# Performance work log

Hardware: AMD Instinct MI355X
Metric: run time of the kernel (lower is better)

## Reference

```python
import jax, jax.numpy as jnp
import numpy as np

B, S, D, H = 4, 2048, 1024, 16
HS = D // H          # head size 64
DF = 4 * D           # ffn hidden 4096
EPS = 1e-5


def _layer_norm(x, g, b):
    mu = jnp.mean(x, axis=-1, keepdims=True)
    var = jnp.var(x, axis=-1, keepdims=True)
    return (x - mu) * jax.lax.rsqrt(var + EPS) * g + b


def setup_inputs() -> dict:
    key = jax.random.key(0)
    ks = jax.random.split(key, 12)
    s_d = 1.0 / np.sqrt(D)
    s_f = 1.0 / np.sqrt(DF)
    return {
        "x": jax.random.normal(ks[0], (B, S, D), jnp.float32),
        # per-head q/k/v projections, batched over heads: [H, D, HS]
        "wq": jax.random.uniform(ks[1], (H, D, HS), jnp.float32, -s_d, s_d),
        "wk": jax.random.uniform(ks[2], (H, D, HS), jnp.float32, -s_d, s_d),
        "wv": jax.random.uniform(ks[3], (H, D, HS), jnp.float32, -s_d, s_d),
        "proj_w": jax.random.uniform(ks[4], (D, D), jnp.float32, -s_d, s_d),
        "proj_b": jax.random.uniform(ks[5], (D,), jnp.float32, -s_d, s_d),
        "ff1_w": jax.random.uniform(ks[6], (D, DF), jnp.float32, -s_d, s_d),
        "ff1_b": jax.random.uniform(ks[7], (DF,), jnp.float32, -s_d, s_d),
        "ff2_w": jax.random.uniform(ks[8], (DF, D), jnp.float32, -s_f, s_f),
        "ff2_b": jax.random.uniform(ks[9], (D,), jnp.float32, -s_f, s_f),
        "ln1_g": jnp.ones((D,), jnp.float32),
        "ln1_b": jnp.zeros((D,), jnp.float32),
        "ln2_g": jnp.ones((D,), jnp.float32),
        "ln2_b": jnp.zeros((D,), jnp.float32),
    }


def reference(x, wq, wk, wv, proj_w, proj_b, ff1_w, ff1_b, ff2_w, ff2_b,
              ln1_g, ln1_b, ln2_g, ln2_b):
    # --- multi-head causal self-attention on ln1(x), all heads batched ---
    h = _layer_norm(x, ln1_g, ln1_b)                      # [B,S,D]
    q = jnp.einsum("bsd,hde->bhse", h, wq)                # [B,H,S,HS]
    k = jnp.einsum("bsd,hde->bhse", h, wk)
    v = jnp.einsum("bsd,hde->bhse", h, wv)
    scale = HS ** -0.5
    scores = jnp.einsum("bhse,bhte->bhst", q, k) * scale  # [B,H,S,S]
    causal = jnp.tril(jnp.ones((S, S), bool))
    scores = jnp.where(causal, scores, jnp.finfo(scores.dtype).min)
    att = jax.nn.softmax(scores, axis=-1)
    o = jnp.einsum("bhst,bhte->bhse", att, v)             # [B,H,S,HS]
    o = o.transpose(0, 2, 1, 3).reshape(B, S, D)          # concat heads
    sa = o @ proj_w + proj_b
    x = x + sa
    # --- FFN on ln2(x) ---
    h2 = _layer_norm(x, ln2_g, ln2_b)
    ff = jax.nn.relu(h2 @ ff1_w + ff1_b) @ ff2_w + ff2_b
    return x + ff
```

## Files before the change

kernel.cpp:

```cpp
#include <hip/hip_runtime.h>
#include <hip/hip_bf16.h>

#define BB 4
#define SS 2048
#define DD 1024
#define HH 16
#define HSZ 64
#define DFF 4096

typedef short short8 __attribute__((ext_vector_type(8)));
typedef float f32x4 __attribute__((ext_vector_type(4)));
typedef unsigned short us4 __attribute__((ext_vector_type(4)));

#define AS1 __attribute__((address_space(1)))
#define AS3 __attribute__((address_space(3)))

__device__ __forceinline__ unsigned short f2bf(float f) {
    return __bfloat16_as_ushort(__float2bfloat16(f));
}

__global__ __launch_bounds__(256) void pack_qkv_kernel(
    const float* __restrict__ wq, const float* __restrict__ wk,
    const float* __restrict__ wv, __hip_bfloat16* __restrict__ out)
{
    int id = blockIdx.x * 256 + threadIdx.x;
    int n = id >> 10;
    int k = id & 1023;
    int sel = n >> 10;
    int hn = n & 1023;
    int h = hn >> 6, e = hn & 63;
    const float* src = (sel == 0) ? wq : (sel == 1) ? wk : wv;
    out[id] = __float2bfloat16(src[(size_t)h * (DD * HSZ) + (size_t)k * HSZ + e]);
}

__global__ __launch_bounds__(256) void pack_T_kernel(
    const float* __restrict__ in, __hip_bfloat16* __restrict__ out, int K, int N)
{
    int id = blockIdx.x * 256 + threadIdx.x;
    int n = id / K;
    int k = id - n * K;
    out[id] = __float2bfloat16(in[(size_t)k * N + n]);
}

__global__ __launch_bounds__(256) void ln_kernel(
    const float* __restrict__ x, const float* __restrict__ g,
    const float* __restrict__ b, __hip_bfloat16* __restrict__ out)
{
    int row = blockIdx.x;
    int t = threadIdx.x;
    const float4* xr = (const float4*)(x + (size_t)row * DD);
    float4 v = xr[t];
    float s = v.x + v.y + v.z + v.w;
    float ss = v.x * v.x + v.y * v.y + v.z * v.z + v.w * v.w;
    #pragma unroll
    for (int off = 32; off; off >>= 1) {
        s += __shfl_xor(s, off, 64);
        ss += __shfl_xor(ss, off, 64);
    }
    __shared__ float red[8];
    int w = t >> 6, lane = t & 63;
    if (lane == 0) { red[w] = s; red[4 + w] = ss; }
    __syncthreads();
    s = red[0] + red[1] + red[2] + red[3];
    ss = red[4] + red[5] + red[6] + red[7];
    float mu = s * (1.f / DD);
    float var = ss * (1.f / DD) - mu * mu;
    float rs = rsqrtf(var + 1e-5f);
    float4 gv = ((const float4*)g)[t];
    float4 bv = ((const float4*)b)[t];
    ushort4 pk = make_ushort4(
        f2bf((v.x - mu) * rs * gv.x + bv.x),
        f2bf((v.y - mu) * rs * gv.y + bv.y),
        f2bf((v.z - mu) * rs * gv.z + bv.z),
        f2bf((v.w - mu) * rs * gv.w + bv.w));
    *(ushort4*)((unsigned short*)out + (size_t)row * DD + t * 4) = pk;
}

template<int BN, bool BIAS, bool RELU, bool RES, bool OUTF32>
__global__ __launch_bounds__(512) void gemm_kernel(
    const __hip_bfloat16* __restrict__ A, const __hip_bfloat16* __restrict__ BT,
    const float* __restrict__ bias, const float* __restrict__ res,
    void* __restrict__ Cout, int M, int N, int K, int nbx)
{
    constexpr int WN = (BN == 256) ? 4 : 2;
    constexpr int MREP = (BN == 256) ? 8 : 4;
    constexpr int BLOADS = BN / 64;
    __shared__ uint4 As[2][2048];
    __shared__ uint4 Bs[2][BN * 8];

    const int t = threadIdx.x;
    const int lane = t & 63, w = t >> 6;
    const int lr = lane & 15, g = lane >> 4;
    const int nwg = gridDim.x;
    const int cpx = nwg >> 3;
    const int wg = blockIdx.x;
    const int swz = (wg & 7) * cpx + (wg >> 3);
    const int bx = swz % nbx, by = swz / nbx;
    const int row0 = by * 256, col0 = bx * BN;
    const int wr = (w / WN) * (MREP * 16), wc = (w % WN) * 64;

    f32x4 acc[MREP][4] = {};
    const int NT = K >> 6;

    auto stage = [&](int buf, int k0) {
        #pragma unroll
        for (int j = 0; j < 4; ++j) {
            int s = j * 512 + t;
            int r = s >> 3;
            int kb = (s & 7) ^ (r & 7);
            const __hip_bfloat16* src = A + (size_t)(row0 + r) * K + k0 + kb * 8;
            __builtin_amdgcn_global_load_lds((const AS1 void*)src,
                (AS3 void*)(&As[buf][j * 512 + (t & ~63)]), 16, 0, 0);
        }
        #pragma unroll
        for (int j = 0; j < BLOADS; ++j) {
            int s = j * 512 + t;
            int r = s >> 3;
            int kb = (s & 7) ^ (r & 7);
            const __hip_bfloat16* src = BT + (size_t)(col0 + r) * K + k0 + kb * 8;
            __builtin_amdgcn_global_load_lds((const AS1 void*)src,
                (AS3 void*)(&Bs[buf][j * 512 + (t & ~63)]), 16, 0, 0);
        }
    };

    auto compute = [&](int buf) {
        short8 bf[4][2];
        #pragma unroll
        for (int n = 0; n < 4; ++n) {
            int c = wc + n * 16 + lr;
            #pragma unroll
            for (int kk = 0; kk < 2; ++kk)
                bf[n][kk] = *(const short8*)&Bs[buf][c * 8 + ((kk * 4 + g) ^ (c & 7))];
        }
        #pragma unroll
        for (int ph = 0; ph < MREP / 2; ++ph) {
            short8 af[2][2];
            #pragma unroll
            for (int m2 = 0; m2 < 2; ++m2) {
                int r = wr + ph * 32 + m2 * 16 + lr;
                #pragma unroll
                for (int kk = 0; kk < 2; ++kk)
                    af[m2][kk] = *(const short8*)&As[buf][r * 8 + ((kk * 4 + g) ^ (r & 7))];
            }
            __builtin_amdgcn_s_setprio(1);
            #pragma unroll
            for (int m2 = 0; m2 < 2; ++m2)
                #pragma unroll
                for (int n = 0; n < 4; ++n)
                    #pragma unroll
                    for (int kk = 0; kk < 2; ++kk)
                        acc[ph * 2 + m2][n] = __builtin_amdgcn_mfma_f32_16x16x32_bf16(
                            af[m2][kk], bf[n][kk], acc[ph * 2 + m2][n], 0, 0, 0);
            __builtin_amdgcn_s_setprio(0);
        }
    };

    stage(0, 0);
    int cur = 0;
    for (int tt = 0; tt < NT - 1; ++tt) {
        stage(cur ^ 1, (tt + 1) * 64);
        if constexpr (BN == 256) asm volatile("s_waitcnt vmcnt(8)" ::: "memory");
        else                     asm volatile("s_waitcnt vmcnt(6)" ::: "memory");
        __builtin_amdgcn_s_barrier();
        compute(cur);
        __builtin_amdgcn_sched_barrier(0);
        __builtin_amdgcn_s_barrier();
        cur ^= 1;
    }
    asm volatile("s_waitcnt vmcnt(0)" ::: "memory");
    __builtin_amdgcn_s_barrier();
    compute(cur);

    #pragma unroll
    for (int mi = 0; mi < MREP; ++mi) {
        #pragma unroll
        for (int j = 0; j < 4; ++j) {
            int rr = row0 + wr + mi * 16 + g * 4 + j;
            #pragma unroll
            for (int n = 0; n < 4; ++n) {
                int cc = col0 + wc + n * 16 + lr;
                float vv = acc[mi][n][j];
                if (BIAS) vv += bias[cc];
                if (RELU) vv = fmaxf(vv, 0.f);
                if (RES) vv += res[(size_t)rr * N + cc];
                if (OUTF32) ((float*)Cout)[(size_t)rr * N + cc] = vv;
                else ((__hip_bfloat16*)Cout)[(size_t)rr * N + cc] = __float2bfloat16(vv);
            }
        }
    }
}

__device__ __forceinline__ void stage_kv(
    const unsigned short* __restrict__ qkvu, size_t rowbase, int h, int kv0, int tl,
    unsigned short* __restrict__ Kb, unsigned short* __restrict__ Vb)
{
    {
        int kv = tl >> 2, c = tl & 3;
        const unsigned short* src = qkvu + rowbase + (size_t)(kv0 + kv) * 3072 + DD + h * HSZ + c * 16;
        uint4 v0 = *(const uint4*)src;
        uint4 v1 = *(const uint4*)(src + 8);
        int sw = kv & 7;
        *(uint4*)&Kb[kv * 64 + ((2 * c) ^ sw) * 8] = v0;
        *(uint4*)&Kb[kv * 64 + ((2 * c + 1) ^ sw) * 8] = v1;
    }
    {
        int bkv = ((tl >> 6) << 2) | (tl & 3);
        int bd = (tl >> 2) & 15;
        const unsigned short* src = qkvu + rowbase + (size_t)(kv0 + bkv * 4) * 3072 + 2 * DD + h * HSZ + bd * 4;
        us4 r0 = *(const us4*)src;
        us4 r1 = *(const us4*)(src + 3072);
        us4 r2 = *(const us4*)(src + 2 * 3072);
        us4 r3 = *(const us4*)(src + 3 * 3072);
        #pragma unroll
        for (int cc = 0; cc < 4; ++cc) {
            int d = bd * 4 + cc;
            us4 wv = { r0[cc], r1[cc], r2[cc], r3[cc] };
            *(us4*)&Vb[d * 64 + (((bkv >> 1) ^ (d & 7)) * 8) + (bkv & 1) * 4] = wv;
        }
    }
}

__device__ __forceinline__ void flash_tile(
    const unsigned short* __restrict__ Kb, const unsigned short* __restrict__ Vb,
    unsigned short* __restrict__ Pw, const short8* qfc, int qgc, int kv0, int q, int g,
    float& m_run, float& l_run, f32x4* oacc)
{
    f32x4 st[4] = {};
    __builtin_amdgcn_s_setprio(1);
    #pragma unroll
    for (int tt = 0; tt < 4; ++tt) {
        #pragma unroll
        for (int kk = 0; kk < 2; ++kk) {
            short8 kf = *(const short8*)&Kb[(tt * 16 + q) * 64 + ((4 * kk + g) ^ (q & 7)) * 8];
            st[tt] = __builtin_amdgcn_mfma_f32_16x16x32_bf16(kf, qfc[kk], st[tt], 0, 0, 0);
        }
    }
    __builtin_amdgcn_s_setprio(0);

    float mt = -1e30f;
    #pragma unroll
    for (int tt = 0; tt < 4; ++tt)
        #pragma unroll
        for (int j = 0; j < 4; ++j) {
            float s = st[tt][j] * 0.125f;
            int kvg = kv0 + tt * 16 + g * 4 + j;
            s = (kvg <= qgc) ? s : -1e30f;
            st[tt][j] = s;
            mt = fmaxf(mt, s);
        }
    mt = fmaxf(mt, __shfl_xor(mt, 16, 64));
    mt = fmaxf(mt, __shfl_xor(mt, 32, 64));
    float m_new = fmaxf(m_run, mt);
    float corr = __expf(m_run - m_new);
    float lsum = 0.f;
    #pragma unroll
    for (int tt = 0; tt < 4; ++tt)
        #pragma unroll
        for (int j = 0; j < 4; ++j) {
            float p = __expf(st[tt][j] - m_new);
            st[tt][j] = p;
            lsum += p;
        }
    lsum += __shfl_xor(lsum, 16, 64);
    lsum += __shfl_xor(lsum, 32, 64);
    l_run = l_run * corr + lsum;
    m_run = m_new;

    #pragma unroll
    for (int tt = 0; tt < 4; ++tt) {
        unsigned int lo = ((unsigned int)f2bf(st[tt][1]) << 16) | (unsigned int)f2bf(st[tt][0]);
        unsigned int hi = ((unsigned int)f2bf(st[tt][3]) << 16) | (unsigned int)f2bf(st[tt][2]);
        uint2 pk = make_uint2(lo, hi);
        *(uint2*)&Pw[q * 64 + ((2 * tt + (g >> 1)) ^ (q & 7)) * 8 + (g & 1) * 4] = pk;
    }

    #pragma unroll
    for (int j = 0; j < 4; ++j) {
        float cj = __shfl(corr, g * 4 + j, 64);
        #pragma unroll
        for (int dn = 0; dn < 4; ++dn)
            oacc[dn][j] *= cj;
    }

    __builtin_amdgcn_s_setprio(1);
    #pragma unroll
    for (int kk = 0; kk < 2; ++kk) {
        short8 pf = *(const short8*)&Pw[q * 64 + ((4 * kk + g) ^ (q & 7)) * 8];
        #pragma unroll
        for (int dn = 0; dn < 4; ++dn) {
            short8 vf = *(const short8*)&Vb[(dn * 16 + q) * 64 + ((4 * kk + g) ^ (q & 7)) * 8];
            oacc[dn] = __builtin_amdgcn_mfma_f32_16x16x32_bf16(pf, vf, oacc[dn], 0, 0, 0);
        }
    }
    __builtin_amdgcn_s_setprio(0);
}

__global__ __launch_bounds__(512) void attn_kernel(
    const __hip_bfloat16* __restrict__ qkv, __hip_bfloat16* __restrict__ o)
{
    __shared__ unsigned short K_lds[2][64 * 64];
    __shared__ unsigned short Vt_lds[2][64 * 64];
    __shared__ unsigned short P_lds[8 * 1024];

    const int t = threadIdx.x;
    const int lane = t & 63, w = t >> 6;
    const int grp = w >> 2, wq4 = w & 3, tl = t & 255;
    const int q = lane & 15, g = lane >> 4;
    const int pq = blockIdx.x & 15;
    const int h = (blockIdx.x >> 4) & 15;
    const int b = blockIdx.x >> 8;
    const int qtA = pq, qtB = 31 - pq;
    const int qt1 = grp ? qtB : qtA;
    const unsigned short* qkvu = (const unsigned short*)qkv;
    const size_t rowbase = (size_t)(b * SS) * 3072;
    unsigned short* Kb = K_lds[grp];
    unsigned short* Vb = Vt_lds[grp];
    unsigned short* Pw = &P_lds[w * 1024];
    unsigned short* op = (unsigned short*)o;

    int qgc = qt1 * 64 + wq4 * 16 + q;
    short8 qfc[2];
    #pragma unroll
    for (int kk = 0; kk < 2; ++kk)
        qfc[kk] = *(const short8*)(qkvu + rowbase + (size_t)qgc * 3072 + h * HSZ + kk * 32 + g * 8);

    f32x4 oacc[4] = {};
    float m_run = -1e30f, l_run = 0.f;

    for (int it = 0; it <= pq; ++it) {
        __syncthreads();
        stage_kv(qkvu, rowbase, h, it * 64, tl, Kb, Vb);
        __syncthreads();
        flash_tile(Kb, Vb, Pw, qfc, qgc, it * 64, q, g, m_run, l_run, oacc);
    }

    if (grp == 0) {
        #pragma unroll
        for (int j = 0; j < 4; ++j) {
            float lj = __shfl(l_run, g * 4 + j, 64);
            float inv = 1.f / lj;
            int orow = qtA * 64 + wq4 * 16 + g * 4 + j;
            #pragma unroll
            for (int dn = 0; dn < 4; ++dn)
                op[(size_t)(b * SS + orow) * DD + h * HSZ + dn * 16 + q] = f2bf(oacc[dn][j] * inv);
        }
        qgc = qtB * 64 + wq4 * 16 + q;
        #pragma unroll
        for (int kk = 0; kk < 2; ++kk)
            qfc[kk] = *(const short8*)(qkvu + rowbase + (size_t)qgc * 3072 + h * HSZ + kk * 32 + g * 8);
        m_run = -1e30f; l_run = 0.f;
        #pragma unroll
        for (int dn = 0; dn < 4; ++dn) oacc[dn] = f32x4{0.f, 0.f, 0.f, 0.f};
    }

    for (int it2 = 0; it2 < 16 - pq; ++it2) {
        int tile = grp ? (pq + 1 + it2) : (16 + it2);
        bool active = grp ? (tile <= 15) : true;
        __syncthreads();
        if (active) stage_kv(qkvu, rowbase, h, tile * 64, tl, Kb, Vb);
        __syncthreads();
        if (active) flash_tile(Kb, Vb, Pw, qfc, qgc, tile * 64, q, g, m_run, l_run, oacc);
    }

    __syncthreads();
    float* obuf = (float*)K_lds;
    float* mlbuf = (float*)P_lds;
    if (grp == 0) {
        #pragma unroll
        for (int dn = 0; dn < 4; ++dn)
            #pragma unroll
            for (int j = 0; j < 4; ++j)
                obuf[wq4 * 1024 + lane * 16 + dn * 4 + j] = oacc[dn][j];
        if (g == 0) { mlbuf[wq4 * 32 + q] = m_run; mlbuf[wq4 * 32 + 16 + q] = l_run; }
    }
    __syncthreads();
    if (grp == 1) {
        float mA = mlbuf[wq4 * 32 + q];
        float lA = mlbuf[wq4 * 32 + 16 + q];
        float mM = fmaxf(m_run, mA);
        float sB = __expf(m_run - mM);
        float sA = __expf(mA - mM);
        float lM = l_run * sB + lA * sA;
        #pragma unroll
        for (int j = 0; j < 4; ++j) {
            float sBj = __shfl(sB, g * 4 + j, 64);
            float sAj = __shfl(sA, g * 4 + j, 64);
            float lMj = __shfl(lM, g * 4 + j, 64);
            float inv = 1.f / lMj;
            int orow = qtB * 64 + wq4 * 16 + g * 4 + j;
            #pragma unroll
            for (int dn = 0; dn < 4; ++dn) {
                float oA = obuf[wq4 * 1024 + lane * 16 + dn * 4 + j];
                float vv = (oacc[dn][j] * sBj + oA * sAj) * inv;
                op[(size_t)(b * SS + orow) * DD + h * HSZ + dn * 16 + q] = f2bf(vv);
            }
        }
    }
}

extern "C" void kernel_launch(void* const* d_in, const int* in_sizes, int n_in,
                              void* d_out, int out_size, void* d_ws, size_t ws_size,
                              hipStream_t stream)
{
    const float* x      = (const float*)d_in[0];
    const float* wq     = (const float*)d_in[1];
    const float* wk     = (const float*)d_in[2];
    const float* wv     = (const float*)d_in[3];
    const float* proj_w = (const float*)d_in[4];
    const float* proj_b = (const float*)d_in[5];
    const float* ff1_w  = (const float*)d_in[6];
    const float* ff1_b  = (const float*)d_in[7];
    const float* ff2_w  = (const float*)d_in[8];
    const float* ff2_b  = (const float*)d_in[9];
    const float* ln1_g  = (const float*)d_in[10];
    const float* ln1_b  = (const float*)d_in[11];
    const float* ln2_g  = (const float*)d_in[12];
    const float* ln2_b  = (const float*)d_in[13];
    float* out = (float*)d_out;

    char* ws = (char*)d_ws;
    const size_t MB = 1ull << 20;
    __hip_bfloat16* h     = (__hip_bfloat16*)(ws);
    __hip_bfloat16* qkv   = (__hip_bfloat16*)(ws + 16 * MB);
    __hip_bfloat16* obuf  = (__hip_bfloat16*)(ws + 64 * MB);
    float*          x1    = (float*)(ws + 80 * MB);
    __hip_bfloat16* wqkvT = (__hip_bfloat16*)(ws + 112 * MB);
    __hip_bfloat16* projT = (__hip_bfloat16*)(ws + 118 * MB);
    __hip_bfloat16* ff1T  = (__hip_bfloat16*)(ws + 120 * MB);
    __hip_bfloat16* ff2T  = (__hip_bfloat16*)(ws + 128 * MB);
    __hip_bfloat16* f1    = (__hip_bfloat16*)(ws + 16 * MB);

    const int ROWS = BB * SS;

    pack_qkv_kernel<<<(3 * DD * DD) / 256, 256, 0, stream>>>(wq, wk, wv, wqkvT);
    pack_T_kernel<<<(DD * DD) / 256, 256, 0, stream>>>(proj_w, projT, DD, DD);
    pack_T_kernel<<<(DD * DFF) / 256, 256, 0, stream>>>(ff1_w, ff1T, DD, DFF);
    pack_T_kernel<<<(DFF * DD) / 256, 256, 0, stream>>>(ff2_w, ff2T, DFF, DD);

    ln_kernel<<<ROWS, 256, 0, stream>>>(x, ln1_g, ln1_b, h);
    gemm_kernel<256, false, false, false, false><<<(ROWS / 256) * (3 * DD / 256), 512, 0, stream>>>(
        h, wqkvT, nullptr, nullptr, qkv, ROWS, 3 * DD, DD, 3 * DD / 256);
    attn_kernel<<<BB * HH * 16, 512, 0, stream>>>(qkv, obuf);
    gemm_kernel<128, true, false, true, true><<<(ROWS / 256) * (DD / 128), 512, 0, stream>>>(
        obuf, projT, proj_b, x, x1, ROWS, DD, DD, DD / 128);
    ln_kernel<<<ROWS, 256, 0, stream>>>(x1, ln2_g, ln2_b, h);
    gemm_kernel<256, true, true, false, false><<<(ROWS / 256) * (DFF / 256), 512, 0, stream>>>(
        h, ff1T, ff1_b, nullptr, f1, ROWS, DFF, DD, DFF / 256);
    gemm_kernel<128, true, false, true, true><<<(ROWS / 256) * (DD / 128), 512, 0, stream>>>(
        f1, ff2T, ff2_b, x1, out, ROWS, DD, DFF, DD / 128);
}
```

Baseline: 441.9 us.

## Split GEMM K-tiles into half-stage LDS buffers for finer-grained load/compute overlap

Each 64-wide K tile of the GEMM is split into two 32-wide halves with separate LDS buffers. Loads for the next half are issued right after each barrier, interleaved with MFMA phases on the current half, so prefetch depth runs at half-tile granularity. The goal is to hide global-to-LDS latency better and keep more loads in flight. In exchange there are twice as many barriers per K tile, and the vmcnt accounting has to stay correct; the last iteration on the shorter NT path is the riskiest part.

```diff
diff --git a/kernel.cpp b/kernel.cpp
--- a/kernel.cpp
+++ b/kernel.cpp
@@ -84,12 +84,12 @@
 {
     constexpr int WN = (BN == 256) ? 4 : 2;
     constexpr int MREP = (BN == 256) ? 8 : 4;
-    constexpr int BLOADS = BN / 64;
-    __shared__ uint4 As[2][2048];
-    __shared__ uint4 Bs[2][BN * 8];
-
-    const int t = threadIdx.x;
-    const int lane = t & 63, w = t >> 6;
+    constexpr int BJ = BN / 128;
+    __shared__ uint4 Ah[2][2][1024];
+    __shared__ uint4 Bh[2][2][BN * 4];
+
+    const int tid = threadIdx.x;
+    const int lane = tid & 63, w = tid >> 6;
     const int lr = lane & 15, g = lane >> 4;
     const int nwg = gridDim.x;
     const int cpx = nwg >> 3;
@@ -102,74 +102,83 @@
     f32x4 acc[MREP][4] = {};
     const int NT = K >> 6;
 
-    auto stage = [&](int buf, int k0) {
-        #pragma unroll
-        for (int j = 0; j < 4; ++j) {
-            int s = j * 512 + t;
-            int r = s >> 3;
-            int kb = (s & 7) ^ (r & 7);
-            const __hip_bfloat16* src = A + (size_t)(row0 + r) * K + k0 + kb * 8;
+    auto stageA = [&](int buf, int kh, int t) {
+        int k0 = t * 64 + kh * 32;
+        #pragma unroll
+        for (int j = 0; j < 2; ++j) {
+            int s = j * 512 + tid;
+            int r = s >> 2;
+            int c2 = (s & 3) ^ (r & 3);
+            const __hip_bfloat16* src = A + (size_t)(row0 + r) * K + k0 + c2 * 8;
             __builtin_amdgcn_global_load_lds((const AS1 void*)src,
-                (AS3 void*)(&As[buf][j * 512 + (t & ~63)]), 16, 0, 0);
-        }
-        #pragma unroll
-        for (int j = 0; j < BLOADS; ++j) {
-            int s = j * 512 + t;
-            int r = s >> 3;
-            int kb = (s & 7) ^ (r & 7);
-            const __hip_bfloat16* src = BT + (size_t)(col0 + r) * K + k0 + kb * 8;
+                (AS3 void*)(&Ah[buf][kh][j * 512 + (tid & ~63)]), 16, 0, 0);
+        }
+    };
+    auto stageB = [&](int buf, int kh, int t) {
+        int k0 = t * 64 + kh * 32;
+        #pragma unroll
+        for (int j = 0; j < BJ; ++j) {
+            int s = j * 512 + tid;
+            int r = s >> 2;
+            int c2 = (s & 3) ^ (r & 3);
+            const __hip_bfloat16* src = BT + (size_t)(col0 + r) * K + k0 + c2 * 8;
             __builtin_amdgcn_global_load_lds((const AS1 void*)src,
-                (AS3 void*)(&Bs[buf][j * 512 + (t & ~63)]), 16, 0, 0);
+                (AS3 void*)(&Bh[buf][kh][j * 512 + (tid & ~63)]), 16, 0, 0);
         }
     };
-
-    auto compute = [&](int buf) {
-        short8 bf[4][2];
+    auto phase = [&](int buf, int kh) {
+        short8 bf[4];
         #pragma unroll
         for (int n = 0; n < 4; ++n) {
             int c = wc + n * 16 + lr;
+            bf[n] = *(const short8*)&Bh[buf][kh][c * 4 + (g ^ (c & 3))];
+        }
+        short8 af[MREP];
+        #pragma unroll
+        for (int mi = 0; mi < MREP; ++mi) {
+            int r = wr + mi * 16 + lr;
+            af[mi] = *(const short8*)&Ah[buf][kh][r * 4 + (g ^ (r & 3))];
+        }
+        __builtin_amdgcn_s_setprio(1);
+        #pragma unroll
+        for (int mi = 0; mi < MREP; ++mi)
             #pragma unroll
-            for (int kk = 0; kk < 2; ++kk)
-                bf[n][kk] = *(const short8*)&Bs[buf][c * 8 + ((kk * 4 + g) ^ (c & 7))];
-        }
-        #pragma unroll
-        for (int ph = 0; ph < MREP / 2; ++ph) {
-            short8 af[2][2];
-            #pragma unroll
-            for (int m2 = 0; m2 < 2; ++m2) {
-                int r = wr + ph * 32 + m2 * 16 + lr;
-                #pragma unroll
-                for (int kk = 0; kk < 2; ++kk)
-                    af[m2][kk] = *(const short8*)&As[buf][r * 8 + ((kk * 4 + g) ^ (r & 7))];
-            }
-            __builtin_amdgcn_s_setprio(1);
-            #pragma unroll
-            for (int m2 = 0; m2 < 2; ++m2)
-                #pragma unroll
-                for (int n = 0; n < 4; ++n)
-                    #pragma unroll
-                    for (int kk = 0; kk < 2; ++kk)
-                        acc[ph * 2 + m2][n] = __builtin_amdgcn_mfma_f32_16x16x32_bf16(
-                            af[m2][kk], bf[n][kk], acc[ph * 2 + m2][n], 0, 0, 0);
-            __builtin_amdgcn_s_setprio(0);
-        }
+            for (int n = 0; n < 4; ++n)
+                acc[mi][n] = __builtin_amdgcn_mfma_f32_16x16x32_bf16(af[mi], bf[n], acc[mi][n], 0, 0, 0);
+        __builtin_amdgcn_s_setprio(0);
     };
 
-    stage(0, 0);
-    int cur = 0;
-    for (int tt = 0; tt < NT - 1; ++tt) {
-        stage(cur ^ 1, (tt + 1) * 64);
+    stageA(0, 0, 0); stageB(0, 0, 0);
+    stageA(0, 1, 0); stageB(0, 1, 0);
+    stageA(1, 0, 1); stageB(1, 0, 1);
+
+    for (int t = 0; t < NT - 1; ++t) {
+        const int buf = t & 1;
         if constexpr (BN == 256) asm volatile("s_waitcnt vmcnt(8)" ::: "memory");
         else                     asm volatile("s_waitcnt vmcnt(6)" ::: "memory");
         __builtin_amdgcn_s_barrier();
-        compute(cur);
         __builtin_amdgcn_sched_barrier(0);
+        stageA(buf ^ 1, 1, t + 1); stageB(buf ^ 1, 1, t + 1);
+        phase(buf, 0);
+        if constexpr (BN == 256) asm volatile("s_waitcnt vmcnt(8)" ::: "memory");
+        else                     asm volatile("s_waitcnt vmcnt(6)" ::: "memory");
         __builtin_amdgcn_s_barrier();
-        cur ^= 1;
-    }
-    asm volatile("s_waitcnt vmcnt(0)" ::: "memory");
-    __builtin_amdgcn_s_barrier();
-    compute(cur);
+        __builtin_amdgcn_sched_barrier(0);
+        if (t < NT - 2) { stageA(buf, 0, t + 2); stageB(buf, 0, t + 2); }
+        phase(buf, 1);
+    }
+    {
+        const int buf = (NT - 1) & 1;
+        if constexpr (BN == 256) asm volatile("s_waitcnt vmcnt(4)" ::: "memory");
+        else                     asm volatile("s_waitcnt vmcnt(3)" ::: "memory");
+        __builtin_amdgcn_s_barrier();
+        __builtin_amdgcn_sched_barrier(0);
+        phase(buf, 0);
+        asm volatile("s_waitcnt vmcnt(0)" ::: "memory");
+        __builtin_amdgcn_s_barrier();
+        __builtin_amdgcn_sched_barrier(0);
+        phase(buf, 1);
+    }
 
     #pragma unroll
     for (int mi = 0; mi < MREP; ++mi) {
```

Measured after the change: 480.6 us. 1.09x slower.
